# Kernel tuning notes

Measured on AMD Instinct MI355X. Metric: run time of the kernel, lower is better.

Reference implementation:

```python
import jax, jax.numpy as jnp
import numpy as np

B, F0, F1, E, C = 256, 39, 39, 16, 1  # batch, feature_nums[0], feature_nums[1], emb_size, w_channels
_ROWS, _COLS = np.tril_indices(F1, k=-1)  # strict lower triangle of (F1, F0); row-major order matches masked_select
I = _ROWS.shape[0]  # interaction_num = 741
BN_EPS = 1e-5


def setup_inputs() -> dict:
    key = jax.random.key(0)
    k1, k2, k3 = jax.random.split(key, 3)
    xi = jax.random.normal(k1, (B, F0, E), dtype=jnp.float32)
    xj = jax.random.normal(k2, (B, F1, E), dtype=jnp.float32)
    # W param is (1,1,C,E,E) in torch; keep the broadcastable core (C,E,E). Xavier-uniform bound.
    bound = float(np.sqrt(6.0 / (E + E)))
    W = jax.random.uniform(k3, (C, E, E), dtype=jnp.float32, minval=-bound, maxval=bound)
    gamma = jnp.ones((I,), dtype=jnp.float32)   # BatchNorm2d weight
    beta = jnp.zeros((I,), dtype=jnp.float32)   # BatchNorm2d bias
    return {"xi": xi, "xj": xj, "W": W, "gamma": gamma, "beta": beta}


def reference(xi, xj, W, gamma, beta):
    rows = jnp.asarray(_ROWS)
    cols = jnp.asarray(_COLS)
    # raw_cross[b,f1,f0,e1,e2] = xj[b,f1,e1] * xi[b,f0,e2]; only keep strict-lower-tri (f1,f0) pairs.
    # Compute triangular pairs directly instead of materializing the full (B,F1,F0,E,E) tensor.
    cross = xj[:, rows, :, None] * xi[:, cols, None, :]  # (B, I, E, E)
    # BatchNorm2d (training-mode batch stats, biased variance) over channels I
    mean = jnp.mean(cross, axis=(0, 2, 3), keepdims=True)            # (1, I, 1, 1)
    var = jnp.mean(jnp.square(cross - mean), axis=(0, 2, 3), keepdims=True)
    normed = (cross - mean) * jax.lax.rsqrt(var + BN_EPS)
    normed = normed * gamma[None, :, None, None] + beta[None, :, None, None]
    # broadcast multiply with W over w_channels, then transpose(1,2)
    out = normed[:, :, None, :, :] * W[None, None, :, :, :]          # (B, I, C, E, E)
    return jnp.transpose(out, (0, 2, 1, 3, 4))                        # (B, C, I, E, E)
```

## Files before the change

### kernel.cpp

```cpp
#include <hip/hip_runtime.h>
#include <math.h>

#define BB 256
#define FF 39
#define EE 16
#define II 741
#define BN_EPS 1e-5f
#define CPW 8
#define NB 8
#define NCX 24
#define NGY (BB / NB)
#define NROW (BB * FF)

typedef float vfloat4 __attribute__((ext_vector_type(4)));
typedef float vfloat2 __attribute__((ext_vector_type(2)));

struct OffTab { unsigned int v[II]; };
static constexpr OffTab make_off() {
    OffTab t{};
    int i = 0;
    for (int r = 1; r < FF; ++r)
        for (int c = 0; c < r; ++c) {
            t.v[i] = ((unsigned)(r * EE) << 16) | (unsigned)(c * EE);
            ++i;
        }
    return t;
}
__constant__ OffTab g_off = make_off();


__global__ void rowsumT_kernel(const float* __restrict__ xi,
                               const float* __restrict__ xj,
                               float* __restrict__ ws) {
    int t = blockIdx.x * blockDim.x + threadIdx.x;
    if (t >= 2 * NROW) return;
    int tensor = (t >= NROW) ? 1 : 0;
    int row = tensor ? (t - NROW) : t;
    int b = row / FF;
    int f = row - b * FF;
    const float* src = (tensor ? xj : xi) + row * EE;
    float s = 0.f, q = 0.f;
#pragma unroll
    for (int k = 0; k < 4; ++k) {
        vfloat4 v = reinterpret_cast<const vfloat4*>(src)[k];
        s += v.x + v.y + v.z + v.w;
        q += v.x * v.x + v.y * v.y + v.z * v.z + v.w * v.w;
    }
    vfloat2* base = reinterpret_cast<vfloat2*>(ws) + (tensor ? NROW : 0);
    vfloat2 e; e.x = s; e.y = q;
    base[f * BB + b] = e;
}

#define LOADB(S, V, b)                                                        \
    {                                                                         \
        const float* xib_ = xi + (b) * FF * EE;                               \
        const float* xjb_ = xj + (b) * FF * EE;                               \
        _Pragma("unroll") for (int k = 0; k < CPW; ++k) {                     \
            S[k] = xjb_[joff[k] + e1];                                        \
            V[k] = reinterpret_cast<const vfloat4*>(xib_ + coff[k])[e2q];     \
        }                                                                     \
    }

#define STOREB(S, V, b)                                                       \
    {                                                                         \
        float* outb_ = out + (size_t)(b) * (II * EE * EE)                     \
                       + (size_t)ibase * (EE * EE);                           \
        _Pragma("unroll") for (int k = 0; k < CPW; ++k) {                     \
            vfloat4 o4;                                                       \
            o4.x = (S[k] * V[k].x * a[k] + d[k]) * w4.x;                      \
            o4.y = (S[k] * V[k].y * a[k] + d[k]) * w4.y;                      \
            o4.z = (S[k] * V[k].z * a[k] + d[k]) * w4.z;                      \
            o4.w = (S[k] * V[k].w * a[k] + d[k]) * w4.w;                      \
            reinterpret_cast<vfloat4*>(outb_ + k * (EE * EE))[l] = o4;        \
        }                                                                     \
    }

__global__ __launch_bounds__(256) void
cross_bn_kernel(const float* __restrict__ xi,
                const float* __restrict__ xj,
                const float* __restrict__ W,
                const float* __restrict__ gamma,
                const float* __restrict__ beta,
                const float* __restrict__ ws,
                float* __restrict__ out) {
    const vfloat2* Ti = reinterpret_cast<const vfloat2*>(ws);
    const vfloat2* Tj = Ti + NROW;

    int t = threadIdx.x;
    int l = t & 63;
    int e1 = l >> 2;
    int e2q = l & 3;
    int wv = t >> 6;

    vfloat4 w4 = reinterpret_cast<const vfloat4*>(W)[e1 * 4 + e2q];

    int ibase = __builtin_amdgcn_readfirstlane(blockIdx.x * (4 * CPW) + wv * CPW);
    int b0 = blockIdx.y * NB;
    int nval = II - ibase;
    if (nval <= 0) return;
    if (nval > CPW) nval = CPW;

    int joff[CPW], coff[CPW];
    float a[CPW], d[CPW];
    const float invN = 1.0f / (float)(BB * EE * EE);
#pragma unroll
    for (int k = 0; k < CPW; ++k) {
        if (k < nval) {
            unsigned o = g_off.v[ibase + k];
            joff[k] = (int)(o >> 16);
            coff[k] = (int)(o & 0xffffu);
            int rb = joff[k] * (BB / EE);
            int cb = coff[k] * (BB / EE);
            float sS = 0.f, sQ = 0.f;
#pragma unroll
            for (int m = 0; m < 4; ++m) {
                int b = l + 64 * m;
                vfloat2 pj = Tj[rb + b];
                vfloat2 pi = Ti[cb + b];
                sS += pj.x * pi.x;
                sQ += pj.y * pi.y;
            }
#pragma unroll
            for (int off = 32; off > 0; off >>= 1) {
                sS += __shfl_xor(sS, off);
                sQ += __shfl_xor(sQ, off);
            }
            float mean = sS * invN;
            float var = sQ * invN - mean * mean;
            float inv_std = 1.0f / sqrtf(var + BN_EPS);
            a[k] = gamma[ibase + k] * inv_std;
            d[k] = beta[ibase + k] - mean * a[k];
        }
    }

    if (nval == CPW) {
        float sA[CPW], sB[CPW];
        vfloat4 vA[CPW], vB[CPW];
        LOADB(sA, vA, b0 + 0)
        LOADB(sB, vB, b0 + 1)
        STOREB(sA, vA, b0 + 0)  LOADB(sA, vA, b0 + 2)
        STOREB(sB, vB, b0 + 1)  LOADB(sB, vB, b0 + 3)
        STOREB(sA, vA, b0 + 2)  LOADB(sA, vA, b0 + 4)
        STOREB(sB, vB, b0 + 3)  LOADB(sB, vB, b0 + 5)
        STOREB(sA, vA, b0 + 4)  LOADB(sA, vA, b0 + 6)
        STOREB(sB, vB, b0 + 5)  LOADB(sB, vB, b0 + 7)
        STOREB(sA, vA, b0 + 6)
        STOREB(sB, vB, b0 + 7)
    } else {
#pragma unroll
        for (int bb = 0; bb < NB; ++bb) {
            int b = b0 + bb;
            const float* xib = xi + b * FF * EE;
            const float* xjb = xj + b * FF * EE;
            float* outb = out + (size_t)b * (II * EE * EE);
            for (int k = 0; k < nval; ++k) {
                int i = ibase + k;
                float xjs = xjb[joff[k] + e1];
                vfloat4 xi4 = reinterpret_cast<const vfloat4*>(xib + coff[k])[e2q];
                vfloat4 o4;
                o4.x = (xjs * xi4.x * a[k] + d[k]) * w4.x;
                o4.y = (xjs * xi4.y * a[k] + d[k]) * w4.y;
                o4.z = (xjs * xi4.z * a[k] + d[k]) * w4.z;
                o4.w = (xjs * xi4.w * a[k] + d[k]) * w4.w;
                reinterpret_cast<vfloat4*>(outb + (size_t)i * (EE * EE))[l] = o4;
            }
        }
    }
}

extern "C" void kernel_launch(void* const* d_in, const int* in_sizes, int n_in,
                              void* d_out, int out_size, void* d_ws, size_t ws_size,
                              hipStream_t stream) {
    const float* xi = (const float*)d_in[0];
    const float* xj = (const float*)d_in[1];
    const float* W = (const float*)d_in[2];
    const float* gamma = (const float*)d_in[3];
    const float* beta = (const float*)d_in[4];
    float* out = (float*)d_out;
    float* ws = (float*)d_ws;

    rowsumT_kernel<<<dim3((2 * NROW + 255) / 256), 256, 0, stream>>>(xi, xj, ws);
    cross_bn_kernel<<<dim3(NCX, NGY), 256, 0, stream>>>(xi, xj, W, gamma, beta, ws, out);
}
```

Measured before the change: 46.37 us.

## Parallelize BN stats across wave lanes and double batches per block

Computes the per-channel BN sums for all 8 channels of a wave at once, with 8 lanes per channel and a short 3-step shuffle reduction, instead of 8 sequential full-wave reductions. The offset table is padded to 768 entries so reads past the last channel stay in bounds. Each block now covers 16 batches instead of 8, halving the redundant stat recomputation per block. The manual load/store software pipeline is replaced by a plain loop unrolled by two, which halves the grid and may reduce occupancy and latency hiding.

New measurement: 53.52 us. 1.15x slower.

```diff
diff --git a/kernel.cpp b/kernel.cpp
--- a/kernel.cpp
+++ b/kernel.cpp
@@ -7,15 +7,16 @@
 #define II 741
 #define BN_EPS 1e-5f
 #define CPW 8
-#define NB 8
+#define NB 16
 #define NCX 24
 #define NGY (BB / NB)
 #define NROW (BB * FF)
+#define BFE (FF * EE)
 
 typedef float vfloat4 __attribute__((ext_vector_type(4)));
 typedef float vfloat2 __attribute__((ext_vector_type(2)));
 
-struct OffTab { unsigned int v[II]; };
+struct OffTab { unsigned int v[768]; };
 static constexpr OffTab make_off() {
     OffTab t{};
     int i = 0;
@@ -24,6 +25,7 @@
             t.v[i] = ((unsigned)(r * EE) << 16) | (unsigned)(c * EE);
             ++i;
         }
+    for (; i < 768; ++i) t.v[i] = 0;
     return t;
 }
 __constant__ OffTab g_off = make_off();
@@ -51,30 +53,6 @@
     base[f * BB + b] = e;
 }
 
-#define LOADB(S, V, b)                                                        \
-    {                                                                         \
-        const float* xib_ = xi + (b) * FF * EE;                               \
-        const float* xjb_ = xj + (b) * FF * EE;                               \
-        _Pragma("unroll") for (int k = 0; k < CPW; ++k) {                     \
-            S[k] = xjb_[joff[k] + e1];                                        \
-            V[k] = reinterpret_cast<const vfloat4*>(xib_ + coff[k])[e2q];     \
-        }                                                                     \
-    }
-
-#define STOREB(S, V, b)                                                       \
-    {                                                                         \
-        float* outb_ = out + (size_t)(b) * (II * EE * EE)                     \
-                       + (size_t)ibase * (EE * EE);                           \
-        _Pragma("unroll") for (int k = 0; k < CPW; ++k) {                     \
-            vfloat4 o4;                                                       \
-            o4.x = (S[k] * V[k].x * a[k] + d[k]) * w4.x;                      \
-            o4.y = (S[k] * V[k].y * a[k] + d[k]) * w4.y;                      \
-            o4.z = (S[k] * V[k].z * a[k] + d[k]) * w4.z;                      \
-            o4.w = (S[k] * V[k].w * a[k] + d[k]) * w4.w;                      \
-            reinterpret_cast<vfloat4*>(outb_ + k * (EE * EE))[l] = o4;        \
-        }                                                                     \
-    }
-
 __global__ __launch_bounds__(256) void
 cross_bn_kernel(const float* __restrict__ xi,
                 const float* __restrict__ xj,
@@ -92,66 +70,80 @@
     int e2q = l & 3;
     int wv = t >> 6;
 
-    vfloat4 w4 = reinterpret_cast<const vfloat4*>(W)[e1 * 4 + e2q];
-
     int ibase = __builtin_amdgcn_readfirstlane(blockIdx.x * (4 * CPW) + wv * CPW);
     int b0 = blockIdx.y * NB;
     int nval = II - ibase;
     if (nval <= 0) return;
     if (nval > CPW) nval = CPW;
 
+    vfloat4 w4 = reinterpret_cast<const vfloat4*>(W)[e1 * 4 + e2q];
+
+    int g = l >> 3;
+    int s = l & 7;
+    {
+    }
+    unsigned og = g_off.v[ibase + g];
+    int rb = (int)(og >> 16) * (BB / EE);
+    int cb = (int)(og & 0xffffu) * (BB / EE);
+
+    float sS = 0.f, sQ = 0.f;
+#pragma unroll
+    for (int m = 0; m < 32; ++m) {
+        int b = s + 8 * m;
+        vfloat2 pj = Tj[rb + b];
+        vfloat2 pi = Ti[cb + b];
+        sS += pj.x * pi.x;
+        sQ += pj.y * pi.y;
+    }
+#pragma unroll
+    for (int off = 1; off < 8; off <<= 1) {
+        sS += __shfl_xor(sS, off);
+        sQ += __shfl_xor(sQ, off);
+    }
+
     int joff[CPW], coff[CPW];
     float a[CPW], d[CPW];
     const float invN = 1.0f / (float)(BB * EE * EE);
 #pragma unroll
     for (int k = 0; k < CPW; ++k) {
-        if (k < nval) {
-            unsigned o = g_off.v[ibase + k];
-            joff[k] = (int)(o >> 16);
-            coff[k] = (int)(o & 0xffffu);
-            int rb = joff[k] * (BB / EE);
-            int cb = coff[k] * (BB / EE);
-            float sS = 0.f, sQ = 0.f;
-#pragma unroll
-            for (int m = 0; m < 4; ++m) {
-                int b = l + 64 * m;
-                vfloat2 pj = Tj[rb + b];
-                vfloat2 pi = Ti[cb + b];
-                sS += pj.x * pi.x;
-                sQ += pj.y * pi.y;
-            }
-#pragma unroll
-            for (int off = 32; off > 0; off >>= 1) {
-                sS += __shfl_xor(sS, off);
-                sQ += __shfl_xor(sQ, off);
-            }
-            float mean = sS * invN;
-            float var = sQ * invN - mean * mean;
-            float inv_std = 1.0f / sqrtf(var + BN_EPS);
-            a[k] = gamma[ibase + k] * inv_std;
-            d[k] = beta[ibase + k] - mean * a[k];
-        }
+        float sSk = __shfl(sS, k * 8);
+        float sQk = __shfl(sQ, k * 8);
+        unsigned ok = g_off.v[ibase + k];
+        joff[k] = (int)(ok >> 16);
+        coff[k] = (int)(ok & 0xffffu);
+        int ii = ibase + k; if (ii > II - 1) ii = II - 1;
+        float mean = sSk * invN;
+        float var = sQk * invN - mean * mean;
+        float inv_std = 1.0f / sqrtf(var + BN_EPS);
+        a[k] = gamma[ii] * inv_std;
+        d[k] = beta[ii] - mean * a[k];
     }
 
     if (nval == CPW) {
-        float sA[CPW], sB[CPW];
-        vfloat4 vA[CPW], vB[CPW];
-        LOADB(sA, vA, b0 + 0)
-        LOADB(sB, vB, b0 + 1)
-        STOREB(sA, vA, b0 + 0)  LOADB(sA, vA, b0 + 2)
-        STOREB(sB, vB, b0 + 1)  LOADB(sB, vB, b0 + 3)
-        STOREB(sA, vA, b0 + 2)  LOADB(sA, vA, b0 + 4)
-        STOREB(sB, vB, b0 + 3)  LOADB(sB, vB, b0 + 5)
-        STOREB(sA, vA, b0 + 4)  LOADB(sA, vA, b0 + 6)
-        STOREB(sB, vB, b0 + 5)  LOADB(sB, vB, b0 + 7)
-        STOREB(sA, vA, b0 + 6)
-        STOREB(sB, vB, b0 + 7)
-    } else {
-#pragma unroll
+#pragma unroll 2
         for (int bb = 0; bb < NB; ++bb) {
             int b = b0 + bb;
-            const float* xib = xi + b * FF * EE;
-            const float* xjb = xj + b * FF * EE;
+            const float* xib = xi + b * BFE;
+            const float* xjb = xj + b * BFE;
+            float* outb = out + (size_t)b * (II * EE * EE)
+                          + (size_t)ibase * (EE * EE);
+#pragma unroll
+            for (int k = 0; k < CPW; ++k) {
+                float xjs = xjb[joff[k] + e1];
+                vfloat4 xi4 = reinterpret_cast<const vfloat4*>(xib + coff[k])[e2q];
+                vfloat4 o4;
+                o4.x = (xjs * xi4.x * a[k] + d[k]) * w4.x;
+                o4.y = (xjs * xi4.y * a[k] + d[k]) * w4.y;
+                o4.z = (xjs * xi4.z * a[k] + d[k]) * w4.z;
+                o4.w = (xjs * xi4.w * a[k] + d[k]) * w4.w;
+                reinterpret_cast<vfloat4*>(outb + k * (EE * EE))[l] = o4;
+            }
+        }
+    } else {
+        for (int bb = 0; bb < NB; ++bb) {
+            int b = b0 + bb;
+            const float* xib = xi + b * BFE;
+            const float* xjb = xj + b * BFE;
             float* outb = out + (size_t)b * (II * EE * EE);
             for (int k = 0; k < nval; ++k) {
                 int i = ibase + k;
```
